# Kernel tuning notes

Measured on AMD Instinct MI355X. Metric: run time of the kernel, lower is better.

The kernel has to match this reference:

```python
import jax, jax.numpy as jnp
import numpy as np

LSTM_DIM = 2048
MEL_DIM = 512
INPUT_SIZE = 512
MAX_STEPS = 512
BATCH = 64


def setup_inputs() -> dict:
    key = jax.random.key(0)
    ks = jax.random.split(key, 9)
    s = 0.02
    return {
        "encoder_output": jax.random.normal(ks[0], (BATCH, 128, INPUT_SIZE), jnp.float32),
        "h0": jax.random.normal(ks[1], (1, BATCH, LSTM_DIM), jnp.float32),
        "c0": jax.random.normal(ks[2], (1, BATCH, LSTM_DIM), jnp.float32),
        "W_ih": jax.random.normal(ks[3], (4 * LSTM_DIM, INPUT_SIZE), jnp.float32) * s,
        "W_hh": jax.random.normal(ks[4], (4 * LSTM_DIM, LSTM_DIM), jnp.float32) * s,
        "b_ih": jax.random.normal(ks[5], (4 * LSTM_DIM,), jnp.float32) * s,
        "b_hh": jax.random.normal(ks[6], (4 * LSTM_DIM,), jnp.float32) * s,
        "W_out": jax.random.normal(ks[7], (MEL_DIM, LSTM_DIM), jnp.float32) * s,
        "b_out": jax.random.normal(ks[8], (MEL_DIM,), jnp.float32) * s,
    }


def reference(encoder_output, h0, c0, W_ih, W_hh, b_ih, b_hh, W_out, b_out):
    # never fires with random weights, so run MAX_STEPS via lax.scan.
    B = encoder_output.shape[0]
    h, c = h0[0], c0[0]                       # [B, H]
    x = jnp.zeros((B, MEL_DIM), encoder_output.dtype)  # initial decoder input
    bias = b_ih + b_hh

    def step(carry, _):
        x, h, c = carry
        gates = x @ W_ih.T + h @ W_hh.T + bias  # [B, 4H]
        i, f, g, o = jnp.split(gates, 4, axis=-1)  # torch gate order i,f,g,o
        c_new = jax.nn.sigmoid(f) * c + jax.nn.sigmoid(i) * jnp.tanh(g)
        h_new = jax.nn.sigmoid(o) * jnp.tanh(c_new)
        y = h_new @ W_out.T + b_out              # [B, mel]
        return (y, h_new, c_new), y

    _, ys = jax.lax.scan(step, (x, h, c), None, length=MAX_STEPS)  # [T, B, mel]
    return jnp.transpose(ys, (1, 0, 2))  # [B, T, mel]
```

## Files before the change

### kernel.cpp

```cpp
#include <hip/hip_runtime.h>

#define HDIM 2048
#define G4   8192
#define NB   64
#define NT   512
#define MEL  512
#define KIN  512
#define NWG  256
#define NBH  (NB * HDIM)

typedef __attribute__((ext_vector_type(8))) short short8;
typedef __attribute__((ext_vector_type(4))) float f32x4;
typedef __attribute__((ext_vector_type(4))) unsigned uint32x4;
typedef __attribute__((ext_vector_type(2))) unsigned uint32x2;

__device__ __forceinline__ unsigned short f2bf(float f){
  union { float f; unsigned u; } v; v.f = f;
  return (unsigned short)((v.u + 0x7fffu + ((v.u >> 16) & 1u)) >> 16);
}
__device__ __forceinline__ float sigm(float x){ return 1.f / (1.f + __expf(-x)); }
__device__ __forceinline__ float tanhfast(float x){ return 1.f - 2.f / (__expf(2.f * x) + 1.f); }

__device__ __forceinline__ f32x4 MF(short8 a, short8 b, f32x4 c){
  return __builtin_amdgcn_mfma_f32_16x16x32_bf16(a, b, c, 0, 0, 0);
}
__device__ __forceinline__ short8 as8(uint32x4 u){
  union { uint32x4 u; short8 s; } x; x.u = u; return x.s;
}
template<bool RING>
__device__ __forceinline__ void ldh(uint32x4& d, const unsigned short* p){
  if constexpr (RING)
    asm volatile("global_load_dwordx4 %0, %1, off"
                 : "=&v"(d) : "v"(p) : "memory");
  else
    asm volatile("global_load_dwordx4 %0, %1, off sc0 sc1"
                 : "=&v"(d) : "v"(p) : "memory");
}
__device__ __forceinline__ uint32x2 ld_bypass2(const unsigned* p){
  uint32x2 r;
  asm volatile("global_load_dwordx2 %0, %1, off sc0 sc1\n\t"
               "s_waitcnt vmcnt(0)"
               : "=v"(r) : "v"(p) : "memory");
  return r;
}

__global__ void convert_kernel(const float* __restrict__ src, unsigned short* __restrict__ dst, int n4){
  int stride = gridDim.x * blockDim.x;
  for (int i = blockIdx.x * blockDim.x + threadIdx.x; i < n4; i += stride){
    const float4 v = *(const float4*)(src + (size_t)i * 4);
    uint2 pk;
    pk.x = (unsigned)f2bf(v.x) | ((unsigned)f2bf(v.y) << 16);
    pk.y = (unsigned)f2bf(v.z) | ((unsigned)f2bf(v.w) << 16);
    *(uint2*)(dst + (size_t)i * 4) = pk;
  }
}

__global__ void beff_kernel(const float* __restrict__ W_ih, const float* __restrict__ b_ih,
                            const float* __restrict__ b_hh, const float* __restrict__ b_out,
                            float* __restrict__ b_eff){
  int r = blockIdx.x;
  int lane = threadIdx.x;
  float acc = 0.f;
  for (int k = lane; k < KIN; k += 64) acc += W_ih[(size_t)r * KIN + k] * b_out[k];
  #pragma unroll
  for (int off = 32; off > 0; off >>= 1) acc += __shfl_down(acc, off, 64);
  if (lane == 0) b_eff[r] = b_ih[r] + b_hh[r] + acc;
}

__global__ void ym1_kernel(const float* __restrict__ Wout, const float* __restrict__ h0,
                           const float* __restrict__ b_out, float* __restrict__ ym1){
  const int b = blockIdx.x;
  const int m = blockIdx.y * 64 + threadIdx.x;
  const float* wr = Wout + (size_t)m * HDIM;
  const float* hr = h0 + (size_t)b * HDIM;
  float a0 = 0.f, a1 = 0.f, a2 = 0.f, a3 = 0.f;
  for (int k = 0; k < HDIM; k += 4){
    const float4 wv = *(const float4*)(wr + k);
    const float4 hv = *(const float4*)(hr + k);
    a0 += wv.x * hv.x; a1 += wv.y * hv.y; a2 += wv.z * hv.z; a3 += wv.w * hv.w;
  }
  ym1[(size_t)b * MEL + m] = a0 + a1 + a2 + a3 + b_out[m];
}

__global__ void corr_kernel(const float* __restrict__ Wih, const float* __restrict__ ym1,
                            float* __restrict__ corr){
  const int r = blockIdx.x;
  const int b = threadIdx.x;
  const float* wr = Wih + (size_t)r * KIN;
  const float* yr = ym1 + (size_t)b * MEL;
  float a0 = 0.f, a1 = 0.f, a2 = 0.f, a3 = 0.f;
  for (int m = 0; m < KIN; m += 4){
    const float4 wv = *(const float4*)(wr + m);
    const float4 yv = *(const float4*)(yr + m);
    a0 += wv.x * yv.x; a1 += wv.y * yv.y; a2 += wv.z * yv.z; a3 += wv.w * yv.w;
  }
  corr[(size_t)r * NB + b] = a0 + a1 + a2 + a3;
}

__global__ __launch_bounds__(256) void weff_gemm(const float* __restrict__ W_ih, const float* __restrict__ W_out,
                                                 const float* __restrict__ W_hh, unsigned short* __restrict__ Weff){
  __shared__ __align__(16) float As[32][68];
  __shared__ __align__(16) float Bs[32][68];
  const int bn = blockIdx.x * 64;
  const int bm = blockIdx.y * 64;
  const int t = threadIdx.x;
  const int tx = t & 15, ty = t >> 4;
  float acc[4][4] = {};
  for (int k0 = 0; k0 < KIN; k0 += 32){
    #pragma unroll
    for (int i = 0; i < 2; i++){
      int f = t + i * 256;
      int row = f >> 3, c4 = (f & 7) * 4;
      const float4 v = *(const float4*)(W_ih + (size_t)(bm + row) * KIN + k0 + c4);
      As[c4 + 0][row] = v.x; As[c4 + 1][row] = v.y; As[c4 + 2][row] = v.z; As[c4 + 3][row] = v.w;
    }
    #pragma unroll
    for (int i = 0; i < 2; i++){
      int f = t + i * 256;
      int kr = f >> 4, c4 = (f & 15) * 4;
      *(float4*)&Bs[kr][c4] = *(const float4*)(W_out + (size_t)(k0 + kr) * HDIM + bn + c4);
    }
    __syncthreads();
    #pragma unroll
    for (int kk = 0; kk < 32; kk++){
      const float4 av = *(const float4*)&As[kk][ty * 4];
      const float4 bv = *(const float4*)&Bs[kk][tx * 4];
      const float ar[4] = {av.x, av.y, av.z, av.w};
      const float br[4] = {bv.x, bv.y, bv.z, bv.w};
      #pragma unroll
      for (int i = 0; i < 4; i++)
        #pragma unroll
        for (int j = 0; j < 4; j++)
          acc[i][j] += ar[i] * br[j];
    }
    __syncthreads();
  }
  #pragma unroll
  for (int i = 0; i < 4; i++){
    const size_t row = (size_t)bm + ty * 4 + i;
    const float4 wh = *(const float4*)(W_hh + row * HDIM + bn + tx * 4);
    uint2 pk;
    pk.x = (unsigned)f2bf(acc[i][0] + wh.x) | ((unsigned)f2bf(acc[i][1] + wh.y) << 16);
    pk.y = (unsigned)f2bf(acc[i][2] + wh.z) | ((unsigned)f2bf(acc[i][3] + wh.w) << 16);
    *(uint2*)(Weff + row * HDIM + bn + tx * 4) = pk;
  }
}

__device__ __forceinline__ void wait128(const unsigned* __restrict__ base, int lane, unsigned tgt){
  const unsigned* sp = base + lane * 2;
  while (true){
    uint32x2 vv = ld_bypass2(sp);
    unsigned m = vv.x < vv.y ? vv.x : vv.y;
    if (__all((int)(m >= tgt))) break;
    __builtin_amdgcn_s_sleep(1);
  }
}

#define LDSX (16384*4 + 512*4)

template<bool RING>
__global__ void __launch_bounds__(512, 1) decoder_coop(
    const unsigned short* __restrict__ Weff_b,
    const unsigned short* __restrict__ Wout_b,
    const float* __restrict__ b_eff,
    const float* __restrict__ corr,
    const float* __restrict__ c0,
    const float* __restrict__ b_out,
    unsigned short* __restrict__ hring,
    unsigned* __restrict__ slots,
    float* __restrict__ out)
{
  extern __shared__ char smem[];
  float* exf = (float*)smem;
  float* eyf = exf + 16384;
  const int bid  = blockIdx.x;
  const int d    = bid & 1;
  const int jg   = bid >> 1;
  const int tid  = threadIdx.x;
  const int v    = tid >> 6;
  const int lane = tid & 63;
  const int col  = lane & 15;
  const int q    = lane >> 4;
  const int kbase = v * 256;

  short8 A0[8], A1[8], A2[8], A3[8], Ay[8];
  #pragma unroll
  for (int it = 0; it < 8; ++it){
    const size_t kc = (size_t)kbase + it * 32 + q * 8;
    A0[it] = *(const short8*)(Weff_b + (size_t)(0 * HDIM + jg * 16 + col) * HDIM + kc);
    A1[it] = *(const short8*)(Weff_b + (size_t)(1 * HDIM + jg * 16 + col) * HDIM + kc);
    A2[it] = *(const short8*)(Weff_b + (size_t)(2 * HDIM + jg * 16 + col) * HDIM + kc);
    A3[it] = *(const short8*)(Weff_b + (size_t)(3 * HDIM + jg * 16 + col) * HDIM + kc);
    if (col < 4)
      Ay[it] = *(const short8*)(Wout_b + (size_t)(jg * 4 + col) * HDIM + kc);
    else { short8 z = {0,0,0,0,0,0,0,0}; Ay[it] = z; }
  }

  const int jl = tid & 15;
  const int bs = tid >> 4;
  const int rj = jg * 16 + jl;
  float be0 = 0.f, be1 = 0.f, be2 = 0.f, be3 = 0.f;
  float cs_s0 = 0.f, cs_s1 = 0.f;
  if (tid < 256){
    be0 = b_eff[0 * HDIM + rj]; be1 = b_eff[1 * HDIM + rj];
    be2 = b_eff[2 * HDIM + rj]; be3 = b_eff[3 * HDIM + rj];
    cs_s0 = c0[(size_t)(d * 32 + bs) * HDIM + rj];
    cs_s1 = c0[(size_t)(d * 32 + 16 + bs) * HDIM + rj];
  }
  const bool isY = (tid >= 256 && tid < 320);
  float byo = 0.f; int yr = 0, ybs = 0;
  if (isY){ const int yt = tid - 256; yr = yt & 3; ybs = yt >> 2; byo = b_out[jg * 4 + yr]; }

  int boff[2];
  #pragma unroll
  for (int s = 0; s < 2; ++s)
    boff[s] = (d * 32 + s * 16 + col) * HDIM + kbase + q * 8;

#define WAITV(N) asm volatile("s_waitcnt vmcnt(" #N ")" ::: "memory"); __builtin_amdgcn_sched_barrier(0);
#define MFM(IT, G) { \
    const short8 bv = as8(G); \
    a0 = MF(A0[IT], bv, a0); a1 = MF(A1[IT], bv, a1); \
    a2 = MF(A2[IT], bv, a2); a3 = MF(A3[IT], bv, a3); \
    ay = MF(Ay[IT], bv, ay); }

  for (int t = 0; t < NT; ++t){
    #pragma unroll
    for (int s = 0; s < 2; ++s){
      unsigned* slot_ds = slots + (d * 2 + s) * 128;
      if (t) wait128(slot_ds, lane, (unsigned)t);

      const unsigned short* hcur = hring + (size_t)(RING ? t : (t & 1)) * NBH;
      const int bo = boff[s];
      uint32x4 G0, G1, G2, G3;
      f32x4 a0 = {0,0,0,0}, a1 = {0,0,0,0}, a2 = {0,0,0,0}, a3 = {0,0,0,0}, ay = {0,0,0,0};

      ldh<RING>(G0, hcur + bo);
      ldh<RING>(G1, hcur + bo + 32);
      ldh<RING>(G2, hcur + bo + 64);
      ldh<RING>(G3, hcur + bo + 96);
      WAITV(3) MFM(0, G0) ldh<RING>(G0, hcur + bo + 128);
      WAITV(3) MFM(1, G1) ldh<RING>(G1, hcur + bo + 160);
      WAITV(3) MFM(2, G2) ldh<RING>(G2, hcur + bo + 192);
      WAITV(3) MFM(3, G3) ldh<RING>(G3, hcur + bo + 224);
      WAITV(3) MFM(4, G0)
      WAITV(2) MFM(5, G1)
      WAITV(1) MFM(6, G2)
      WAITV(0) MFM(7, G3)

      #pragma unroll
      for (int e = 0; e < 4; ++e){
        const int lr = q * 4 + e;
        const int cx = col ^ ((lr & 7) << 2);
        exf[(v * 64 +  0 + lr) * 32 + cx] = a0[e];
        exf[(v * 64 + 16 + lr) * 32 + cx] = a1[e];
        exf[(v * 64 + 32 + lr) * 32 + cx] = a2[e];
        exf[(v * 64 + 48 + lr) * 32 + cx] = a3[e];
      }
      if (q == 0){
        #pragma unroll
        for (int e = 0; e < 4; ++e) eyf[(v * 4 + e) * 16 + col] = ay[e];
      }
      __syncthreads();

      if (tid < 256){
        const int cidx = bs ^ ((jl & 7) << 2);
        float gi = 0.f, gf = 0.f, gg = 0.f, go = 0.f;
        #pragma unroll
        for (int vv = 0; vv < 8; ++vv){
          gi += exf[(vv * 64 +  0 + jl) * 32 + cidx];
          gf += exf[(vv * 64 + 16 + jl) * 32 + cidx];
          gg += exf[(vv * 64 + 32 + jl) * 32 + cidx];
          go += exf[(vv * 64 + 48 + jl) * 32 + cidx];
        }
        const int b = d * 32 + s * 16 + bs;
        gi += be0; gf += be1; gg += be2; go += be3;
        if (t == 0){
          gi -= corr[(size_t)(0 * HDIM + rj) * NB + b];
          gf -= corr[(size_t)(1 * HDIM + rj) * NB + b];
          gg -= corr[(size_t)(2 * HDIM + rj) * NB + b];
          go -= corr[(size_t)(3 * HDIM + rj) * NB + b];
        }
        float cs = s ? cs_s1 : cs_s0;
        const float i_ = sigm(gi), f_ = sigm(gf), g_ = tanhfast(gg), o_ = sigm(go);
        cs = f_ * cs + i_ * g_;
        const float hn = o_ * tanhfast(cs);
        if (s) cs_s1 = cs; else cs_s0 = cs;

        const float pn = __shfl_xor(hn, 1, 64);
        unsigned short* hdst = hring + (size_t)(RING ? (t + 1) : ((t + 1) & 1)) * NBH;
        if ((jl & 1) == 0){
          const unsigned pk = (unsigned)f2bf(hn) | ((unsigned)f2bf(pn) << 16);
          __hip_atomic_store((unsigned*)(hdst + (size_t)b * HDIM + rj), pk,
                             __ATOMIC_RELAXED, __HIP_MEMORY_SCOPE_AGENT);
        }
      } else if (isY && t >= 1){
        float yv = byo;
        #pragma unroll
        for (int vv = 0; vv < 8; ++vv) yv += eyf[(vv * 4 + yr) * 16 + ybs];
        const int b = d * 32 + s * 16 + ybs;
        out[((size_t)b * NT + (t - 1)) * MEL + jg * 4 + yr] = yv;
      }
      __syncthreads();
      if (tid == 0)
        __hip_atomic_store(slot_ds + jg, (unsigned)(t + 1),
                           __ATOMIC_RELAXED, __HIP_MEMORY_SCOPE_AGENT);
    }
  }

  #pragma unroll
  for (int s = 0; s < 2; ++s){
    wait128(slots + (d * 2 + s) * 128, lane, (unsigned)NT);
    const unsigned short* hfin = hring + (size_t)(RING ? NT : 0) * NBH;
    const int bo = boff[s];
    f32x4 ay = {0,0,0,0};
    #pragma unroll
    for (int it = 0; it < 8; ++it){
      uint32x4 g;
      ldh<RING>(g, hfin + bo + it * 32);
      asm volatile("s_waitcnt vmcnt(0)" ::: "memory");
      __builtin_amdgcn_sched_barrier(0);
      ay = MF(Ay[it], as8(g), ay);
    }
    if (q == 0){
      #pragma unroll
      for (int e = 0; e < 4; ++e) eyf[(v * 4 + e) * 16 + col] = ay[e];
    }
    __syncthreads();
    if (isY){
      float yv = byo;
      #pragma unroll
      for (int vv = 0; vv < 8; ++vv) yv += eyf[(vv * 4 + yr) * 16 + ybs];
      const int b = d * 32 + s * 16 + ybs;
      out[((size_t)b * NT + 511) * MEL + jg * 4 + yr] = yv;
    }
    __syncthreads();
  }
}

extern "C" void kernel_launch(void* const* d_in, const int* in_sizes, int n_in,
                              void* d_out, int out_size, void* d_ws, size_t ws_size,
                              hipStream_t stream){
  (void)in_sizes; (void)n_in; (void)out_size;
  const float* h0    = (const float*)d_in[1];
  const float* c0    = (const float*)d_in[2];
  const float* W_ih  = (const float*)d_in[3];
  const float* W_hh  = (const float*)d_in[4];
  const float* b_ih  = (const float*)d_in[5];
  const float* b_hh  = (const float*)d_in[6];
  const float* W_out = (const float*)d_in[7];
  const float* b_out = (const float*)d_in[8];
  float* out = (float*)d_out;

  const size_t fixed = (size_t)G4 * HDIM * 2
                     + (size_t)MEL * HDIM * 2
                     + (size_t)G4 * 4
                     + (size_t)G4 * NB * 4
                     + (size_t)NB * MEL * 4
                     + 4 * 128 * sizeof(unsigned)
                     + 1024;
  const bool ring = ws_size >= fixed + (size_t)(NT + 1) * NBH * 2;
  const int hslots = ring ? (NT + 1) : 2;

  char* p = (char*)d_ws;
  unsigned short* weff_b = (unsigned short*)p; p += (size_t)G4 * HDIM * 2;
  unsigned short* wout_b = (unsigned short*)p; p += (size_t)MEL * HDIM * 2;
  float* beff = (float*)p;  p += (size_t)G4 * 4;
  float* corr = (float*)p;  p += (size_t)G4 * NB * 4;
  float* ym1  = (float*)p;  p += (size_t)NB * MEL * 4;
  unsigned* slots = (unsigned*)p; p += 4 * 128 * sizeof(unsigned);
  unsigned short* hring = (unsigned short*)p; p += (size_t)hslots * NBH * 2;

  hipMemsetAsync(slots, 0, 4 * 128 * sizeof(unsigned), stream);
  convert_kernel<<<256, 256, 0, stream>>>(W_out, wout_b, MEL * HDIM / 4);
  convert_kernel<<<64, 256, 0, stream>>>(h0, hring, NBH / 4);
  beff_kernel<<<G4, 64, 0, stream>>>(W_ih, b_ih, b_hh, b_out, beff);
  ym1_kernel<<<dim3(NB, MEL / 64), 64, 0, stream>>>(W_out, h0, b_out, ym1);
  corr_kernel<<<G4, NB, 0, stream>>>(W_ih, ym1, corr);
  weff_gemm<<<dim3(HDIM / 64, G4 / 64), 256, 0, stream>>>(W_ih, W_out, W_hh, weff_b);

  void* kargs[] = { (void*)&weff_b, (void*)&wout_b, (void*)&beff, (void*)&corr,
                    (void*)&c0, (void*)&b_out, (void*)&hring, (void*)&slots, (void*)&out };
  if (ring){
    hipFuncSetAttribute((const void*)decoder_coop<true>,
                        hipFuncAttributeMaxDynamicSharedMemorySize, LDSX);
    hipLaunchCooperativeKernel((const void*)decoder_coop<true>, dim3(NWG), dim3(512),
                               kargs, LDSX, stream);
  } else {
    hipFuncSetAttribute((const void*)decoder_coop<false>,
                        hipFuncAttributeMaxDynamicSharedMemorySize, LDSX);
    hipLaunchCooperativeKernel((const void*)decoder_coop<false>, dim3(NWG), dim3(512),
                               kargs, LDSX, stream);
  }
}
```

Before: 4.396 ms.

## Publish per-wave readiness flags instead of per-workgroup flag after barrier

Result: faster. 4.039 ms (-8.1%).

```diff
diff --git a/kernel.cpp b/kernel.cpp
--- a/kernel.cpp
+++ b/kernel.cpp
@@ -8,11 +8,11 @@
 #define KIN  512
 #define NWG  256
 #define NBH  (NB * HDIM)
+#define NSLOT 512
 
 typedef __attribute__((ext_vector_type(8))) short short8;
 typedef __attribute__((ext_vector_type(4))) float f32x4;
 typedef __attribute__((ext_vector_type(4))) unsigned uint32x4;
-typedef __attribute__((ext_vector_type(2))) unsigned uint32x2;
 
 __device__ __forceinline__ unsigned short f2bf(float f){
   union { float f; unsigned u; } v; v.f = f;
@@ -35,13 +35,6 @@
   else
     asm volatile("global_load_dwordx4 %0, %1, off sc0 sc1"
                  : "=&v"(d) : "v"(p) : "memory");
-}
-__device__ __forceinline__ uint32x2 ld_bypass2(const unsigned* p){
-  uint32x2 r;
-  asm volatile("global_load_dwordx2 %0, %1, off sc0 sc1\n\t"
-               "s_waitcnt vmcnt(0)"
-               : "=v"(r) : "v"(p) : "memory");
-  return r;
 }
 
 __global__ void convert_kernel(const float* __restrict__ src, unsigned short* __restrict__ dst, int n4){
@@ -146,12 +139,23 @@
   }
 }
 
-__device__ __forceinline__ void wait128(const unsigned* __restrict__ base, int lane, unsigned tgt){
-  const unsigned* sp = base + lane * 2;
+__device__ __forceinline__ void wait512(const unsigned* __restrict__ base, int lane, unsigned tgt){
+  const unsigned* sp = base + lane * 8;
   while (true){
-    uint32x2 vv = ld_bypass2(sp);
-    unsigned m = vv.x < vv.y ? vv.x : vv.y;
-    if (__all((int)(m >= tgt))) break;
+    uint32x4 a, b;
+    asm volatile("global_load_dwordx4 %0, %2, off sc0 sc1\n\t"
+                 "global_load_dwordx4 %1, %3, off sc0 sc1\n\t"
+                 "s_waitcnt vmcnt(0)"
+                 : "=&v"(a), "=&v"(b)
+                 : "v"(sp), "v"(sp + 4) : "memory");
+    unsigned m0 = a.x < a.y ? a.x : a.y;
+    unsigned m1 = a.z < a.w ? a.z : a.w;
+    unsigned m2 = b.x < b.y ? b.x : b.y;
+    unsigned m3 = b.z < b.w ? b.z : b.w;
+    m0 = m0 < m1 ? m0 : m1;
+    m2 = m2 < m3 ? m2 : m3;
+    m0 = m0 < m2 ? m0 : m2;
+    if (__all((int)(m0 >= tgt))) break;
     __builtin_amdgcn_s_sleep(1);
   }
 }
@@ -226,8 +230,8 @@
   for (int t = 0; t < NT; ++t){
     #pragma unroll
     for (int s = 0; s < 2; ++s){
-      unsigned* slot_ds = slots + (d * 2 + s) * 128;
-      if (t) wait128(slot_ds, lane, (unsigned)t);
+      unsigned* slot_ds = slots + (d * 2 + s) * NSLOT;
+      if (t) wait512(slot_ds, lane, (unsigned)t);
 
       const unsigned short* hcur = hring + (size_t)(RING ? t : (t & 1)) * NBH;
       const int bo = boff[s];
@@ -246,6 +250,8 @@
       WAITV(2) MFM(5, G1)
       WAITV(1) MFM(6, G2)
       WAITV(0) MFM(7, G3)
+
+      __syncthreads();
 
       #pragma unroll
       for (int e = 0; e < 4; ++e){
@@ -293,6 +299,11 @@
           __hip_atomic_store((unsigned*)(hdst + (size_t)b * HDIM + rj), pk,
                              __ATOMIC_RELAXED, __HIP_MEMORY_SCOPE_AGENT);
         }
+        asm volatile("s_waitcnt vmcnt(0)" ::: "memory");
+        __builtin_amdgcn_sched_barrier(0);
+        if (lane == 0)
+          __hip_atomic_store(slot_ds + (jg << 2) + v, (unsigned)(t + 1),
+                             __ATOMIC_RELAXED, __HIP_MEMORY_SCOPE_AGENT);
       } else if (isY && t >= 1){
         float yv = byo;
         #pragma unroll
@@ -300,16 +311,12 @@
         const int b = d * 32 + s * 16 + ybs;
         out[((size_t)b * NT + (t - 1)) * MEL + jg * 4 + yr] = yv;
       }
-      __syncthreads();
-      if (tid == 0)
-        __hip_atomic_store(slot_ds + jg, (unsigned)(t + 1),
-                           __ATOMIC_RELAXED, __HIP_MEMORY_SCOPE_AGENT);
     }
   }
 
   #pragma unroll
   for (int s = 0; s < 2; ++s){
-    wait128(slots + (d * 2 + s) * 128, lane, (unsigned)NT);
+    wait512(slots + (d * 2 + s) * NSLOT, lane, (unsigned)NT);
     const unsigned short* hfin = hring + (size_t)(RING ? NT : 0) * NBH;
     const int bo = boff[s];
     f32x4 ay = {0,0,0,0};
@@ -321,6 +328,7 @@
       __builtin_amdgcn_sched_barrier(0);
       ay = MF(Ay[it], as8(g), ay);
     }
+    __syncthreads();
     if (q == 0){
       #pragma unroll
       for (int e = 0; e < 4; ++e) eyf[(v * 4 + e) * 16 + col] = ay[e];
@@ -356,7 +364,7 @@
                      + (size_t)G4 * 4
                      + (size_t)G4 * NB * 4
                      + (size_t)NB * MEL * 4
-                     + 4 * 128 * sizeof(unsigned)
+                     + 4 * NSLOT * sizeof(unsigned)
                      + 1024;
   const bool ring = ws_size >= fixed + (size_t)(NT + 1) * NBH * 2;
   const int hslots = ring ? (NT + 1) : 2;
@@ -367,10 +375,10 @@
   float* beff = (float*)p;  p += (size_t)G4 * 4;
   float* corr = (float*)p;  p += (size_t)G4 * NB * 4;
   float* ym1  = (float*)p;  p += (size_t)NB * MEL * 4;
-  unsigned* slots = (unsigned*)p; p += 4 * 128 * sizeof(unsigned);
+  unsigned* slots = (unsigned*)p; p += 4 * NSLOT * sizeof(unsigned);
   unsigned short* hring = (unsigned short*)p; p += (size_t)hslots * NBH * 2;
 
-  hipMemsetAsync(slots, 0, 4 * 128 * sizeof(unsigned), stream);
+  hipMemsetAsync(slots, 0, 4 * NSLOT * sizeof(unsigned), stream);
   convert_kernel<<<256, 256, 0, stream>>>(W_out, wout_b, MEL * HDIM / 4);
   convert_kernel<<<64, 256, 0, stream>>>(h0, hring, NBH / 4);
   beff_kernel<<<G4, 64, 0, stream>>>(W_ih, b_ih, b_hh, b_out, beff);
```

## Merge both batch halves per timestep to halve cross-workgroup sync rounds

Applied to the files above, without the earlier changes.

Result: slower. 8.566 ms (+94.9%).

```diff
diff --git a/kernel.cpp b/kernel.cpp
--- a/kernel.cpp
+++ b/kernel.cpp
@@ -156,7 +156,7 @@
   }
 }
 
-#define LDSX (16384*4 + 512*4)
+#define LDSX (16384*4 + 1024*4)
 
 template<bool RING>
 __global__ void __launch_bounds__(512, 1) decoder_coop(
@@ -199,141 +199,160 @@
   const int jl = tid & 15;
   const int bs = tid >> 4;
   const int rj = jg * 16 + jl;
-  float be0 = 0.f, be1 = 0.f, be2 = 0.f, be3 = 0.f;
-  float cs_s0 = 0.f, cs_s1 = 0.f;
-  if (tid < 256){
-    be0 = b_eff[0 * HDIM + rj]; be1 = b_eff[1 * HDIM + rj];
-    be2 = b_eff[2 * HDIM + rj]; be3 = b_eff[3 * HDIM + rj];
-    cs_s0 = c0[(size_t)(d * 32 + bs) * HDIM + rj];
-    cs_s1 = c0[(size_t)(d * 32 + 16 + bs) * HDIM + rj];
-  }
-  const bool isY = (tid >= 256 && tid < 320);
-  float byo = 0.f; int yr = 0, ybs = 0;
-  if (isY){ const int yt = tid - 256; yr = yt & 3; ybs = yt >> 2; byo = b_out[jg * 4 + yr]; }
-
-  int boff[2];
-  #pragma unroll
-  for (int s = 0; s < 2; ++s)
-    boff[s] = (d * 32 + s * 16 + col) * HDIM + kbase + q * 8;
+  const int bglob = d * 32 + bs;
+  const float be0 = b_eff[0 * HDIM + rj], be1 = b_eff[1 * HDIM + rj];
+  const float be2 = b_eff[2 * HDIM + rj], be3 = b_eff[3 * HDIM + rj];
+  float cs = c0[(size_t)bglob * HDIM + rj];
+  const float byo = (jl < 4) ? b_out[jg * 4 + jl] : 0.f;
+
+  const int bo0 = (d * 32 + col) * HDIM + kbase + q * 8;
+  const int bo1 = (d * 32 + 16 + col) * HDIM + kbase + q * 8;
 
 #define WAITV(N) asm volatile("s_waitcnt vmcnt(" #N ")" ::: "memory"); __builtin_amdgcn_sched_barrier(0);
-#define MFM(IT, G) { \
+#define MFM0(IT, G) { \
     const short8 bv = as8(G); \
-    a0 = MF(A0[IT], bv, a0); a1 = MF(A1[IT], bv, a1); \
-    a2 = MF(A2[IT], bv, a2); a3 = MF(A3[IT], bv, a3); \
-    ay = MF(Ay[IT], bv, ay); }
+    a00 = MF(A0[IT], bv, a00); a01 = MF(A1[IT], bv, a01); \
+    a02 = MF(A2[IT], bv, a02); a03 = MF(A3[IT], bv, a03); \
+    ay0 = MF(Ay[IT], bv, ay0); }
+#define MFM1(IT, G) { \
+    const short8 bv = as8(G); \
+    a10 = MF(A0[IT], bv, a10); a11 = MF(A1[IT], bv, a11); \
+    a12 = MF(A2[IT], bv, a12); a13 = MF(A3[IT], bv, a13); \
+    ay1 = MF(Ay[IT], bv, ay1); }
+
+  unsigned* slot_d = slots + d * 128;
 
   for (int t = 0; t < NT; ++t){
+    if (t) wait128(slot_d, lane, (unsigned)t);
+
+    const unsigned short* hcur = hring + (size_t)(RING ? t : (t & 1)) * NBH;
+    uint32x4 G0, G1, G2, G3, H0, H1, H2, H3;
+    f32x4 a00 = {0,0,0,0}, a01 = {0,0,0,0}, a02 = {0,0,0,0}, a03 = {0,0,0,0}, ay0 = {0,0,0,0};
+    f32x4 a10 = {0,0,0,0}, a11 = {0,0,0,0}, a12 = {0,0,0,0}, a13 = {0,0,0,0}, ay1 = {0,0,0,0};
+
+    ldh<RING>(G0, hcur + bo0);
+    ldh<RING>(G1, hcur + bo0 + 32);
+    ldh<RING>(G2, hcur + bo0 + 64);
+    ldh<RING>(G3, hcur + bo0 + 96);
+    WAITV(3) MFM0(0, G0) ldh<RING>(G0, hcur + bo0 + 128);
+    WAITV(3) MFM0(1, G1) ldh<RING>(G1, hcur + bo0 + 160);
+    WAITV(3) MFM0(2, G2) ldh<RING>(G2, hcur + bo0 + 192);
+    WAITV(3) MFM0(3, G3) ldh<RING>(G3, hcur + bo0 + 224);
+    ldh<RING>(H0, hcur + bo1);
+    ldh<RING>(H1, hcur + bo1 + 32);
+    ldh<RING>(H2, hcur + bo1 + 64);
+    ldh<RING>(H3, hcur + bo1 + 96);
+    WAITV(7) MFM0(4, G0)
+    WAITV(6) MFM0(5, G1)
+    WAITV(5) MFM0(6, G2)
+    WAITV(4) MFM0(7, G3)
+    WAITV(3) MFM1(0, H0) ldh<RING>(H0, hcur + bo1 + 128);
+    WAITV(3) MFM1(1, H1) ldh<RING>(H1, hcur + bo1 + 160);
+    WAITV(3) MFM1(2, H2) ldh<RING>(H2, hcur + bo1 + 192);
+    WAITV(3) MFM1(3, H3) ldh<RING>(H3, hcur + bo1 + 224);
+    WAITV(3) MFM1(4, H0)
+    WAITV(2) MFM1(5, H1)
+    WAITV(1) MFM1(6, H2)
+    WAITV(0) MFM1(7, H3)
+
+    __syncthreads();
+
     #pragma unroll
-    for (int s = 0; s < 2; ++s){
-      unsigned* slot_ds = slots + (d * 2 + s) * 128;
-      if (t) wait128(slot_ds, lane, (unsigned)t);
-
-      const unsigned short* hcur = hring + (size_t)(RING ? t : (t & 1)) * NBH;
-      const int bo = boff[s];
-      uint32x4 G0, G1, G2, G3;
-      f32x4 a0 = {0,0,0,0}, a1 = {0,0,0,0}, a2 = {0,0,0,0}, a3 = {0,0,0,0}, ay = {0,0,0,0};
-
-      ldh<RING>(G0, hcur + bo);
-      ldh<RING>(G1, hcur + bo + 32);
-      ldh<RING>(G2, hcur + bo + 64);
-      ldh<RING>(G3, hcur + bo + 96);
-      WAITV(3) MFM(0, G0) ldh<RING>(G0, hcur + bo + 128);
-      WAITV(3) MFM(1, G1) ldh<RING>(G1, hcur + bo + 160);
-      WAITV(3) MFM(2, G2) ldh<RING>(G2, hcur + bo + 192);
-      WAITV(3) MFM(3, G3) ldh<RING>(G3, hcur + bo + 224);
-      WAITV(3) MFM(4, G0)
-      WAITV(2) MFM(5, G1)
-      WAITV(1) MFM(6, G2)
-      WAITV(0) MFM(7, G3)
-
+    for (int e = 0; e < 4; ++e){
+      const int lr = q * 4 + e;
+      const int sw = (lr & 7) << 2;
+      const int c0x = col ^ sw;
+      const int c1x = (16 + col) ^ sw;
+      exf[(v * 64 +  0 + lr) * 32 + c0x] = a00[e];
+      exf[(v * 64 + 16 + lr) * 32 + c0x] = a01[e];
+      exf[(v * 64 + 32 + lr) * 32 + c0x] = a02[e];
+      exf[(v * 64 + 48 + lr) * 32 + c0x] = a03[e];
+      exf[(v * 64 +  0 + lr) * 32 + c1x] = a10[e];
+      exf[(v * 64 + 16 + lr) * 32 + c1x] = a11[e];
+      exf[(v * 64 + 32 + lr) * 32 + c1x] = a12[e];
+      exf[(v * 64 + 48 + lr) * 32 + c1x] = a13[e];
+    }
+    if (q == 0){
       #pragma unroll
       for (int e = 0; e < 4; ++e){
-        const int lr = q * 4 + e;
-        const int cx = col ^ ((lr & 7) << 2);
-        exf[(v * 64 +  0 + lr) * 32 + cx] = a0[e];
-        exf[(v * 64 + 16 + lr) * 32 + cx] = a1[e];
-        exf[(v * 64 + 32 + lr) * 32 + cx] = a2[e];
-        exf[(v * 64 + 48 + lr) * 32 + cx] = a3[e];
+        eyf[(v * 4 + e) * 32 + col]      = ay0[e];
+        eyf[(v * 4 + e) * 32 + 16 + col] = ay1[e];
       }
-      if (q == 0){
-        #pragma unroll
-        for (int e = 0; e < 4; ++e) eyf[(v * 4 + e) * 16 + col] = ay[e];
+    }
+    __syncthreads();
+
+    {
+      const int cidx = bs ^ ((jl & 7) << 2);
+      float gi = 0.f, gf = 0.f, gg = 0.f, go = 0.f;
+      #pragma unroll
+      for (int vv = 0; vv < 8; ++vv){
+        gi += exf[(vv * 64 +  0 + jl) * 32 + cidx];
+        gf += exf[(vv * 64 + 16 + jl) * 32 + cidx];
+        gg += exf[(vv * 64 + 32 + jl) * 32 + cidx];
+        go += exf[(vv * 64 + 48 + jl) * 32 + cidx];
       }
-      __syncthreads();
-
-      if (tid < 256){
-        const int cidx = bs ^ ((jl & 7) << 2);
-        float gi = 0.f, gf = 0.f, gg = 0.f, go = 0.f;
-        #pragma unroll
-        for (int vv = 0; vv < 8; ++vv){
-          gi += exf[(vv * 64 +  0 + jl) * 32 + cidx];
-          gf += exf[(vv * 64 + 16 + jl) * 32 + cidx];
-          gg += exf[(vv * 64 + 32 + jl) * 32 + cidx];
-          go += exf[(vv * 64 + 48 + jl) * 32 + cidx];
-        }
-        const int b = d * 32 + s * 16 + bs;
-        gi += be0; gf += be1; gg += be2; go += be3;
-        if (t == 0){
-          gi -= corr[(size_t)(0 * HDIM + rj) * NB + b];
-          gf -= corr[(size_t)(1 * HDIM + rj) * NB + b];
-          gg -= corr[(size_t)(2 * HDIM + rj) * NB + b];
-          go -= corr[(size_t)(3 * HDIM + rj) * NB + b];
-        }
-        float cs = s ? cs_s1 : cs_s0;
-        const float i_ = sigm(gi), f_ = sigm(gf), g_ = tanhfast(gg), o_ = sigm(go);
-        cs = f_ * cs + i_ * g_;
-        const float hn = o_ * tanhfast(cs);
-        if (s) cs_s1 = cs; else cs_s0 = cs;
-
-        const float pn = __shfl_xor(hn, 1, 64);
-        unsigned short* hdst = hring + (size_t)(RING ? (t + 1) : ((t + 1) & 1)) * NBH;
-        if ((jl & 1) == 0){
-          const unsigned pk = (unsigned)f2bf(hn) | ((unsigned)f2bf(pn) << 16);
-          __hip_atomic_store((unsigned*)(hdst + (size_t)b * HDIM + rj), pk,
-                             __ATOMIC_RELAXED, __HIP_MEMORY_SCOPE_AGENT);
-        }
-      } else if (isY && t >= 1){
-        float yv = byo;
-        #pragma unroll
-        for (int vv = 0; vv < 8; ++vv) yv += eyf[(vv * 4 + yr) * 16 + ybs];
-        const int b = d * 32 + s * 16 + ybs;
-        out[((size_t)b * NT + (t - 1)) * MEL + jg * 4 + yr] = yv;
+      gi += be0; gf += be1; gg += be2; go += be3;
+      if (t == 0){
+        gi -= corr[(size_t)(0 * HDIM + rj) * NB + bglob];
+        gf -= corr[(size_t)(1 * HDIM + rj) * NB + bglob];
+        gg -= corr[(size_t)(2 * HDIM + rj) * NB + bglob];
+        go -= corr[(size_t)(3 * HDIM + rj) * NB + bglob];
       }
-      __syncthreads();
-      if (tid == 0)
-        __hip_atomic_store(slot_ds + jg, (unsigned)(t + 1),
+      const float i_ = sigm(gi), f_ = sigm(gf), g_ = tanhfast(gg), o_ = sigm(go);
+      cs = f_ * cs + i_ * g_;
+      const float hn = o_ * tanhfast(cs);
+
+      const float pn = __shfl_xor(hn, 1, 64);
+      unsigned short* hdst = hring + (size_t)(RING ? (t + 1) : ((t + 1) & 1)) * NBH;
+      if ((jl & 1) == 0){
+        const unsigned pk = (unsigned)f2bf(hn) | ((unsigned)f2bf(pn) << 16);
+        __hip_atomic_store((unsigned*)(hdst + (size_t)bglob * HDIM + rj), pk,
                            __ATOMIC_RELAXED, __HIP_MEMORY_SCOPE_AGENT);
-    }
-  }
-
-  #pragma unroll
-  for (int s = 0; s < 2; ++s){
-    wait128(slots + (d * 2 + s) * 128, lane, (unsigned)NT);
+      }
+      asm volatile("s_waitcnt vmcnt(0)" ::: "memory");
+    }
+    __syncthreads();
+    if (tid == 0)
+      __hip_atomic_store(slot_d + jg, (unsigned)(t + 1),
+                         __ATOMIC_RELAXED, __HIP_MEMORY_SCOPE_AGENT);
+
+    if (jl < 4 && t >= 1){
+      float yv = byo;
+      #pragma unroll
+      for (int vv = 0; vv < 8; ++vv) yv += eyf[(vv * 4 + jl) * 32 + bs];
+      out[((size_t)bglob * NT + (t - 1)) * MEL + jg * 4 + jl] = yv;
+    }
+  }
+
+  {
+    wait128(slot_d, lane, (unsigned)NT);
     const unsigned short* hfin = hring + (size_t)(RING ? NT : 0) * NBH;
-    const int bo = boff[s];
-    f32x4 ay = {0,0,0,0};
+    f32x4 ay0 = {0,0,0,0}, ay1 = {0,0,0,0};
     #pragma unroll
     for (int it = 0; it < 8; ++it){
-      uint32x4 g;
-      ldh<RING>(g, hfin + bo + it * 32);
+      uint32x4 g, h;
+      ldh<RING>(g, hfin + bo0 + it * 32);
+      ldh<RING>(h, hfin + bo1 + it * 32);
       asm volatile("s_waitcnt vmcnt(0)" ::: "memory");
       __builtin_amdgcn_sched_barrier(0);
-      ay = MF(Ay[it], as8(g), ay);
-    }
+      ay0 = MF(Ay[it], as8(g), ay0);
+      ay1 = MF(Ay[it], as8(h), ay1);
+    }
+    __syncthreads();
     if (q == 0){
       #pragma unroll
-      for (int e = 0; e < 4; ++e) eyf[(v * 4 + e) * 16 + col] = ay[e];
-    }
-    __syncthreads();
-    if (isY){
+      for (int e = 0; e < 4; ++e){
+        eyf[(v * 4 + e) * 32 + col]      = ay0[e];
+        eyf[(v * 4 + e) * 32 + 16 + col] = ay1[e];
+      }
+    }
+    __syncthreads();
+    if (jl < 4){
       float yv = byo;
       #pragma unroll
-      for (int vv = 0; vv < 8; ++vv) yv += eyf[(vv * 4 + yr) * 16 + ybs];
-      const int b = d * 32 + s * 16 + ybs;
-      out[((size_t)b * NT + 511) * MEL + jg * 4 + yr] = yv;
-    }
-    __syncthreads();
+      for (int vv = 0; vv < 8; ++vv) yv += eyf[(vv * 4 + jl) * 32 + bs];
+      out[((size_t)bglob * NT + 511) * MEL + jg * 4 + jl] = yv;
+    }
   }
 }
 
@@ -356,7 +375,7 @@
                      + (size_t)G4 * 4
                      + (size_t)G4 * NB * 4
                      + (size_t)NB * MEL * 4
-                     + 4 * 128 * sizeof(unsigned)
+                     + 2 * 128 * sizeof(unsigned)
                      + 1024;
   const bool ring = ws_size >= fixed + (size_t)(NT + 1) * NBH * 2;
   const int hslots = ring ? (NT + 1) : 2;
@@ -367,10 +386,10 @@
   float* beff = (float*)p;  p += (size_t)G4 * 4;
   float* corr = (float*)p;  p += (size_t)G4 * NB * 4;
   float* ym1  = (float*)p;  p += (size_t)NB * MEL * 4;
-  unsigned* slots = (unsigned*)p; p += 4 * 128 * sizeof(unsigned);
+  unsigned* slots = (unsigned*)p; p += 2 * 128 * sizeof(unsigned);
   unsigned short* hring = (unsigned short*)p; p += (size_t)hslots * NBH * 2;
 
-  hipMemsetAsync(slots, 0, 4 * 128 * sizeof(unsigned), stream);
+  hipMemsetAsync(slots, 0, 2 * 128 * sizeof(unsigned), stream);
   convert_kernel<<<256, 256, 0, stream>>>(W_out, wout_b, MEL * HDIM / 4);
   convert_kernel<<<64, 256, 0, stream>>>(h0, hring, NBH / 4);
   beff_kernel<<<G4, 64, 0, stream>>>(W_ih, b_ih, b_hh, b_out, beff);
```
